# Kernel optimization log

Hardware: AMD Instinct MI355X
Metric: run time of the kernel (lower is better)

## Reference

```python
import jax, jax.numpy as jnp
import numpy as np

DQ_RATIO, DV_RATIO = 8, 2


def setup_inputs() -> dict:
    key = jax.random.key(0)
    k1, k2, k3, k4 = jax.random.split(key, 4)
    B, C, H, W = 16, 256, 64, 64
    dq, dv = C // DQ_RATIO, C // DV_RATIO
    imgs = jax.random.normal(k1, (B, C, H, W), dtype=jnp.float32)
    # small init keeps softmax logits in a sane range (like trained conv weights)
    w_qkv = jax.random.normal(k2, (2 * dq + dv, C), dtype=jnp.float32) * 0.02
    w_out = jax.random.normal(k3, (C, dv), dtype=jnp.float32) * 0.05
    scale = jax.random.normal(k4, (), dtype=jnp.float32)
    return {"imgs": imgs, "w_qkv": w_qkv, "w_out": w_out, "scale": scale}


def _maxpool2(x):
    # 2x2 max pool, stride 2; x: [b, c, h, w]
    b, c, h, w = x.shape
    return x.reshape(b, c, h // 2, 2, w // 2, 2).max(axis=(3, 5))


def reference(imgs, w_qkv, w_out, scale):
    b, c, h, w = imgs.shape
    dq, dv = c // DQ_RATIO, c // DV_RATIO
    # 1x1 conv == per-pixel channel matmul
    qkv = jnp.einsum('bchw,oc->bohw', imgs, w_qkv)
    q = qkv[:, :dq]                 # [b, dq, h, w]
    k = _maxpool2(qkv[:, dq:2 * dq])  # [b, dq, h/2, w/2]
    v = _maxpool2(qkv[:, 2 * dq:])    # [b, dv, h/2, w/2]
    q = q.reshape(b, dq, h * w)
    k = k.reshape(b, dq, (h * w) // 4)
    v = v.reshape(b, dv, (h * w) // 4)
    # attn[b, n, m] over downsampled kv positions m
    attn = jax.nn.softmax(jnp.einsum('bdn,bdm->bnm', q, k), axis=2)
    out = jnp.einsum('bdm,bnm->bdn', v, attn).reshape(b, dv, h, w)
    return imgs + jnp.einsum('bdhw,cd->bchw', out, w_out) * scale
```

## Files before the change

### kernel.cpp

```cpp
#include <hip/hip_runtime.h>

typedef __bf16 bf16;
typedef __bf16 bf16x2 __attribute__((ext_vector_type(2)));
typedef __bf16 bf16x4 __attribute__((ext_vector_type(4)));
typedef __bf16 bf16x8 __attribute__((ext_vector_type(8)));
typedef float f32x4 __attribute__((ext_vector_type(4)));

#define NB 16
#define NC 256
#define NHW 4096
#define NDQ 32
#define NDV 128
#define NM 1024

__global__ __launch_bounds__(256) void cvt_weights(const float* __restrict__ wq,
                                                   const float* __restrict__ wo,
                                                   bf16* __restrict__ wq16,
                                                   bf16* __restrict__ wo16) {
    int idx = blockIdx.x * 256 + threadIdx.x;
    const float* src;
    bf16* dst;
    int base;
    if (idx < 6144) { src = wq; dst = wq16; base = idx; }
    else            { src = wo; dst = wo16; base = idx - 6144; }
    float4 a = ((const float4*)src)[base * 2];
    float4 c = ((const float4*)src)[base * 2 + 1];
    bf16x8 v;
    v[0] = (bf16)a.x; v[1] = (bf16)a.y; v[2] = (bf16)a.z; v[3] = (bf16)a.w;
    v[4] = (bf16)c.x; v[5] = (bf16)c.y; v[6] = (bf16)c.z; v[7] = (bf16)c.w;
    *(bf16x8*)&dst[base * 8] = v;
}

__global__ __launch_bounds__(256) void qkv_mfma(const float* __restrict__ imgs,
                                                const bf16* __restrict__ wq16,
                                                bf16* __restrict__ qT,
                                                bf16* __restrict__ kT,
                                                bf16* __restrict__ vb) {
    __shared__ __align__(16) char lds[40960];
    bf16* XS = (bf16*)lds;
    bf16* WS = (bf16*)(lds + 16384);

    const int tid  = threadIdx.x;
    const int lane = tid & 63;
    const int w    = tid >> 6;
    const int lr   = lane & 15;
    const int lg   = lane >> 4;
    const int bx   = blockIdx.x;
    const int b    = blockIdx.y;
    const int n0   = bx * 128;

    f32x4 acc[3][8];
#pragma unroll
    for (int i = 0; i < 3; i++)
#pragma unroll
        for (int j = 0; j < 8; j++) acc[i][j] = (f32x4){0.f, 0.f, 0.f, 0.f};

    const int snl = tid & 63;
    const int scg = (tid >> 6) * 8;

    for (int kc = 0; kc < 4; kc++) {
        if (kc) __syncthreads();
#pragma unroll
        for (int j = 0; j < 4; j++) {
            int n  = snl + (j & 1) * 64;
            int c8 = scg + (j >> 1) * 32;
            const float* g = imgs + (size_t)(b * NC + kc * 64 + c8) * NHW + n0 + n;
            bf16x8 v;
#pragma unroll
            for (int i = 0; i < 8; i++) v[i] = (bf16)g[i * NHW];
            *(bf16x8*)(XS + n * 64 + ((((c8 >> 3) ^ (n & 7))) << 3)) = v;
        }
#pragma unroll
        for (int j = 0; j < 6; j++) {
            int idx = j * 256 + tid;
            int o = idx >> 3, s = idx & 7;
            bf16x8 v = *(const bf16x8*)(wq16 + (size_t)o * NC + kc * 64 + s * 8);
            *(bf16x8*)(WS + o * 64 + ((s ^ (o & 7)) << 3)) = v;
        }
        __syncthreads();
#pragma unroll
        for (int sub = 0; sub < 2; sub++) {
            bf16x8 af[3], bfr[8];
#pragma unroll
            for (int ot = 0; ot < 3; ot++) {
                int o = w * 48 + ot * 16 + lr;
                af[ot] = *(const bf16x8*)(WS + o * 64 + (((sub * 4 + lg) ^ (o & 7)) << 3));
            }
#pragma unroll
            for (int nt = 0; nt < 8; nt++) {
                int n = nt * 16 + lr;
                bfr[nt] = *(const bf16x8*)(XS + n * 64 + (((sub * 4 + lg) ^ (n & 7)) << 3));
            }
#pragma unroll
            for (int ot = 0; ot < 3; ot++)
#pragma unroll
                for (int nt = 0; nt < 8; nt++)
                    acc[ot][nt] = __builtin_amdgcn_mfma_f32_16x16x32_bf16(af[ot], bfr[nt], acc[ot][nt], 0, 0, 0);
        }
    }

#pragma unroll
    for (int ot = 0; ot < 3; ot++) {
        const int o_base = w * 48 + ot * 16;
        if (o_base < 32) {
            const int d0 = o_base + lg * 4;
#pragma unroll
            for (int nt = 0; nt < 8; nt++) {
                int n = n0 + nt * 16 + lr;
                bf16x4 v;
#pragma unroll
                for (int r = 0; r < 4; r++) v[r] = (bf16)acc[ot][nt][r];
                *(bf16x4*)&qT[((size_t)b * NHW + n) * NDQ + d0] = v;
            }
        } else {
            float pm[4][4];
#pragma unroll
            for (int ntg = 0; ntg < 4; ntg++)
#pragma unroll
                for (int r = 0; r < 4; r++) {
                    float v0 = fmaxf(acc[ot][ntg][r], acc[ot][ntg + 4][r]);
                    float v1 = __shfl_xor(v0, 1, 64);
                    pm[ntg][r] = fmaxf(v0, v1);
                }
            if (!(lr & 1)) {
                if (o_base < 64) {
                    const int d0 = o_base - 32 + lg * 4;
#pragma unroll
                    for (int ntg = 0; ntg < 4; ntg++) {
                        int m = bx * 32 + ((ntg * 16 + lr) >> 1);
                        bf16x4 v;
#pragma unroll
                        for (int r = 0; r < 4; r++) v[r] = (bf16)pm[ntg][r];
                        *(bf16x4*)&kT[((size_t)b * NM + m) * NDQ + d0] = v;
                    }
                } else {
                    const int dv0 = o_base - 64 + lg * 4;
#pragma unroll
                    for (int ntg = 0; ntg < 4; ntg++) {
                        int m = bx * 32 + ((ntg * 16 + lr) >> 1);
#pragma unroll
                        for (int r = 0; r < 4; r++)
                            vb[((size_t)b * NDV + dv0 + r) * NM + m] = (bf16)pm[ntg][r];
                    }
                }
            }
        }
    }
}

__global__ __launch_bounds__(256) void attn_mfma(const bf16* __restrict__ qT,
                                                 const bf16* __restrict__ kT,
                                                 const bf16* __restrict__ vb,
                                                 bf16* __restrict__ aT) {
    __shared__ __align__(16) char pool[37888];
    bf16* QT = (bf16*)pool;
    bf16* KT = (bf16*)(pool + 5120);
    bf16* VS = (bf16*)(pool + 10240);
    bf16* PS = (bf16*)(pool + 28672);
    float* DW = (float*)(pool + 28672);

    const int tid  = threadIdx.x;
    const int lane = tid & 63;
    const int w    = tid >> 6;
    const int lr   = lane & 15;
    const int lg   = lane >> 4;
    const int b    = blockIdx.y;
    const int n0   = blockIdx.x * 64;

    {
        const bf16* src = qT + (size_t)(b * NHW + n0 + (tid >> 2)) * NDQ + (tid & 3) * 8;
        *(bf16x8*)&QT[(tid >> 2) * 40 + (tid & 3) * 8] = *(const bf16x8*)src;
    }
    __syncthreads();

    bf16x8 QB[4];
#pragma unroll
    for (int nt = 0; nt < 4; nt++)
        QB[nt] = *(const bf16x8*)&QT[(nt * 16 + lr) * 40 + lg * 8];

    f32x4 zero = {0.f, 0.f, 0.f, 0.f};
    f32x4 acc[2][4];
#pragma unroll
    for (int dt = 0; dt < 2; dt++)
#pragma unroll
        for (int nt = 0; nt < 4; nt++) acc[dt][nt] = zero;
    float denp[4] = {0.f, 0.f, 0.f, 0.f};

    for (int t = 0; t < 16; t++) {
        const int m0 = t * 64;
        __syncthreads();
        {
            const bf16* src = kT + (size_t)(b * NM + m0 + (tid >> 2)) * NDQ + (tid & 3) * 8;
            *(bf16x8*)&KT[(tid >> 2) * 40 + (tid & 3) * 8] = *(const bf16x8*)src;
        }
        {
            const bf16* src = vb + (size_t)(b * NDV + (tid >> 1)) * NM + m0 + (tid & 1) * 32;
            bf16* dst = &VS[(tid >> 1) * 72 + (tid & 1) * 32];
#pragma unroll
            for (int u = 0; u < 4; u++)
                *(bf16x8*)(dst + u * 8) = *(const bf16x8*)(src + u * 8);
        }
        __syncthreads();

        bf16x8 ka = *(const bf16x8*)&KT[(w * 16 + lr) * 40 + lg * 8];
        f32x4 st[4];
#pragma unroll
        for (int nt = 0; nt < 4; nt++)
            st[nt] = __builtin_amdgcn_mfma_f32_16x16x32_bf16(ka, QB[nt], zero, 0, 0, 0);

#pragma unroll
        for (int nt = 0; nt < 4; nt++) {
            float e0 = __expf(st[nt][0]);
            float e1 = __expf(st[nt][1]);
            float e2 = __expf(st[nt][2]);
            float e3 = __expf(st[nt][3]);
            denp[nt] += (e0 + e1) + (e2 + e3);
            bf16x4 pv;
            pv[0] = (bf16)e0; pv[1] = (bf16)e1; pv[2] = (bf16)e2; pv[3] = (bf16)e3;
            *(bf16x4*)&PS[(nt * 16 + lr) * 72 + (w * 16 + lg * 4)] = pv;
        }
        __syncthreads();

#pragma unroll
        for (int mc = 0; mc < 2; mc++) {
            bf16x8 pb[4];
#pragma unroll
            for (int nt = 0; nt < 4; nt++)
                pb[nt] = *(const bf16x8*)&PS[(nt * 16 + lr) * 72 + mc * 32 + lg * 8];
#pragma unroll
            for (int dt = 0; dt < 2; dt++) {
                bf16x8 va = *(const bf16x8*)&VS[(w * 32 + dt * 16 + lr) * 72 + mc * 32 + lg * 8];
#pragma unroll
                for (int nt = 0; nt < 4; nt++)
                    acc[dt][nt] = __builtin_amdgcn_mfma_f32_16x16x32_bf16(va, pb[nt], acc[dt][nt], 0, 0, 0);
            }
        }
    }
    __syncthreads();

#pragma unroll
    for (int nt = 0; nt < 4; nt++) {
        denp[nt] += __shfl_xor(denp[nt], 16, 64);
        denp[nt] += __shfl_xor(denp[nt], 32, 64);
    }
    if (lane < 16) {
#pragma unroll
        for (int nt = 0; nt < 4; nt++) DW[(w * 4 + nt) * 16 + lane] = denp[nt];
    }
    __syncthreads();
    float rinv[4];
#pragma unroll
    for (int nt = 0; nt < 4; nt++) {
        float s = DW[(0 * 4 + nt) * 16 + lr] + DW[(1 * 4 + nt) * 16 + lr] +
                  DW[(2 * 4 + nt) * 16 + lr] + DW[(3 * 4 + nt) * 16 + lr];
        rinv[nt] = 1.0f / s;
    }

#pragma unroll
    for (int dt = 0; dt < 2; dt++)
#pragma unroll
        for (int nt = 0; nt < 4; nt++) {
            int d0 = w * 32 + dt * 16 + lg * 4;
            int n  = n0 + nt * 16 + lr;
            bf16x4 v;
#pragma unroll
            for (int r = 0; r < 4; r++) v[r] = (bf16)(acc[dt][nt][r] * rinv[nt]);
            *(bf16x4*)&aT[((size_t)b * NHW + n) * NDV + d0] = v;
        }
}

__global__ __launch_bounds__(256) void outproj_mfma(const bf16* __restrict__ aT,
                                                    const bf16* __restrict__ wo16,
                                                    const float* __restrict__ imgs,
                                                    const float* __restrict__ scale_p,
                                                    float* __restrict__ out) {
    __shared__ __align__(16) char lds[65536];
    bf16* XS = (bf16*)lds;
    bf16* WS = (bf16*)(lds + 32768);

    const int tid  = threadIdx.x;
    const int lane = tid & 63;
    const int w    = tid >> 6;
    const int lr   = lane & 15;
    const int lg   = lane >> 4;
    const int wr   = w >> 1, wc = w & 1;
    const int bx   = blockIdx.x;
    const int ch   = blockIdx.y;
    const int b    = blockIdx.z;
    const int n0   = bx * 128;

#pragma unroll
    for (int j = 0; j < 8; j++) {
        int idx = j * 256 + tid;
        int row = idx >> 4, s = idx & 15;
        int sw  = ((s ^ (row & 15)) << 3);
        *(bf16x8*)(XS + row * 128 + sw) =
            *(const bf16x8*)(aT + ((size_t)b * NHW + n0 + row) * NDV + s * 8);
        *(bf16x8*)(WS + row * 128 + sw) =
            *(const bf16x8*)(wo16 + (size_t)(ch * 128 + row) * NDV + s * 8);
    }
    __syncthreads();

    f32x4 acc[4][4];
#pragma unroll
    for (int i = 0; i < 4; i++)
#pragma unroll
        for (int j = 0; j < 4; j++) acc[i][j] = (f32x4){0.f, 0.f, 0.f, 0.f};

#pragma unroll
    for (int kk = 0; kk < 4; kk++) {
        bf16x8 af[4], bfr[4];
#pragma unroll
        for (int ot = 0; ot < 4; ot++) {
            int c = wr * 64 + ot * 16 + lr;
            af[ot] = *(const bf16x8*)(WS + c * 128 + (((kk * 4 + lg) ^ (c & 15)) << 3));
        }
#pragma unroll
        for (int nt = 0; nt < 4; nt++) {
            int n = wc * 64 + nt * 16 + lr;
            bfr[nt] = *(const bf16x8*)(XS + n * 128 + (((kk * 4 + lg) ^ (n & 15)) << 3));
        }
#pragma unroll
        for (int ot = 0; ot < 4; ot++)
#pragma unroll
            for (int nt = 0; nt < 4; nt++)
                acc[ot][nt] = __builtin_amdgcn_mfma_f32_16x16x32_bf16(af[ot], bfr[nt], acc[ot][nt], 0, 0, 0);
    }

    const float sc = *scale_p;
#pragma unroll
    for (int ot = 0; ot < 4; ot++)
#pragma unroll
        for (int nt = 0; nt < 4; nt++) {
            int n = n0 + wc * 64 + nt * 16 + lr;
#pragma unroll
            for (int r = 0; r < 4; r++) {
                int c = ch * 128 + wr * 64 + ot * 16 + lg * 4 + r;
                size_t off = ((size_t)b * NC + c) * NHW + n;
                out[off] = imgs[off] + sc * acc[ot][nt][r];
            }
        }
}

extern "C" void kernel_launch(void* const* d_in, const int* in_sizes, int n_in,
                              void* d_out, int out_size, void* d_ws, size_t ws_size,
                              hipStream_t stream) {
    const float* imgs  = (const float*)d_in[0];
    const float* w_qkv = (const float*)d_in[1];
    const float* w_out = (const float*)d_in[2];
    const float* scale = (const float*)d_in[3];
    float* out = (float*)d_out;

    char* wsb = (char*)d_ws;
    bf16* aTg  = (bf16*)(wsb);
    bf16* qTg  = (bf16*)(wsb + (16u << 20));
    bf16* kTg  = (bf16*)(wsb + (20u << 20));
    bf16* vbg  = (bf16*)(wsb + (21u << 20));
    bf16* wq16 = (bf16*)(wsb + (25u << 20));
    bf16* wo16 = (bf16*)(wsb + (25u << 20) + 98304);

    hipLaunchKernelGGL(cvt_weights, dim3(40), dim3(256), 0, stream,
                       w_qkv, w_out, wq16, wo16);
    hipLaunchKernelGGL(qkv_mfma, dim3(32, NB), dim3(256), 0, stream,
                       imgs, wq16, qTg, kTg, vbg);
    hipLaunchKernelGGL(attn_mfma, dim3(64, NB), dim3(256), 0, stream,
                       qTg, kTg, vbg, aTg);
    hipLaunchKernelGGL(outproj_mfma, dim3(32, 2, NB), dim3(256), 0, stream,
                       aTg, wo16, imgs, scale, out);
}
```

Before: 181.9 us.

## Retile qkv and attention kernels, prefetch K/V tiles into registers

The qkv projection kernel now covers 64 pixels per block (two half-row slices paired for the 2x2 pool), which doubles its grid for more parallelism and halves its accumulator registers. The attention kernel now handles 128 query pixels per block, so each K/V tile loaded is reused across twice as many queries. It also prefetches the next K/V tile into registers while the current one is computed, hiding global load latency. The costs are more LDS and registers in the attention kernel, which may lower occupancy, and fewer attention blocks.

```diff
diff --git a/kernel.cpp b/kernel.cpp
--- a/kernel.cpp
+++ b/kernel.cpp
@@ -36,9 +36,9 @@
                                                 bf16* __restrict__ qT,
                                                 bf16* __restrict__ kT,
                                                 bf16* __restrict__ vb) {
-    __shared__ __align__(16) char lds[40960];
+    __shared__ __align__(16) char lds[32768];
     bf16* XS = (bf16*)lds;
-    bf16* WS = (bf16*)(lds + 16384);
+    bf16* WS = (bf16*)(lds + 8192);
 
     const int tid  = threadIdx.x;
     const int lane = tid & 63;
@@ -46,29 +46,33 @@
     const int lr   = lane & 15;
     const int lg   = lane >> 4;
     const int bx   = blockIdx.x;
+    const int r    = bx >> 1;
+    const int half = bx & 1;
     const int b    = blockIdx.y;
-    const int n0   = bx * 128;
-
-    f32x4 acc[3][8];
+    const int nfb  = r * 128 + half * 32;
+
+    f32x4 acc[3][4];
 #pragma unroll
     for (int i = 0; i < 3; i++)
 #pragma unroll
-        for (int j = 0; j < 8; j++) acc[i][j] = (f32x4){0.f, 0.f, 0.f, 0.f};
+        for (int j = 0; j < 4; j++) acc[i][j] = (f32x4){0.f, 0.f, 0.f, 0.f};
 
     const int snl = tid & 63;
+    const int sg  = snl >> 5;
+    const int sc  = snl & 31;
     const int scg = (tid >> 6) * 8;
 
     for (int kc = 0; kc < 4; kc++) {
         if (kc) __syncthreads();
 #pragma unroll
-        for (int j = 0; j < 4; j++) {
-            int n  = snl + (j & 1) * 64;
-            int c8 = scg + (j >> 1) * 32;
-            const float* g = imgs + (size_t)(b * NC + kc * 64 + c8) * NHW + n0 + n;
+        for (int j = 0; j < 2; j++) {
+            int c8 = scg + j * 32;
+            const float* g = imgs + (size_t)(b * NC + kc * 64 + c8) * NHW
+                             + nfb + sg * 64 + sc;
             bf16x8 v;
 #pragma unroll
             for (int i = 0; i < 8; i++) v[i] = (bf16)g[i * NHW];
-            *(bf16x8*)(XS + n * 64 + ((((c8 >> 3) ^ (n & 7))) << 3)) = v;
+            *(bf16x8*)(XS + snl * 64 + ((((c8 >> 3) ^ (snl & 7))) << 3)) = v;
         }
 #pragma unroll
         for (int j = 0; j < 6; j++) {
@@ -80,21 +84,21 @@
         __syncthreads();
 #pragma unroll
         for (int sub = 0; sub < 2; sub++) {
-            bf16x8 af[3], bfr[8];
+            bf16x8 af[3], bfr[4];
 #pragma unroll
             for (int ot = 0; ot < 3; ot++) {
                 int o = w * 48 + ot * 16 + lr;
                 af[ot] = *(const bf16x8*)(WS + o * 64 + (((sub * 4 + lg) ^ (o & 7)) << 3));
             }
 #pragma unroll
-            for (int nt = 0; nt < 8; nt++) {
+            for (int nt = 0; nt < 4; nt++) {
                 int n = nt * 16 + lr;
                 bfr[nt] = *(const bf16x8*)(XS + n * 64 + (((sub * 4 + lg) ^ (n & 7)) << 3));
             }
 #pragma unroll
             for (int ot = 0; ot < 3; ot++)
 #pragma unroll
-                for (int nt = 0; nt < 8; nt++)
+                for (int nt = 0; nt < 4; nt++)
                     acc[ot][nt] = __builtin_amdgcn_mfma_f32_16x16x32_bf16(af[ot], bfr[nt], acc[ot][nt], 0, 0, 0);
         }
     }
@@ -105,42 +109,42 @@
         if (o_base < 32) {
             const int d0 = o_base + lg * 4;
 #pragma unroll
-            for (int nt = 0; nt < 8; nt++) {
-                int n = n0 + nt * 16 + lr;
+            for (int nt = 0; nt < 4; nt++) {
+                int n = nfb + (nt >> 1) * 64 + (nt & 1) * 16 + lr;
                 bf16x4 v;
 #pragma unroll
-                for (int r = 0; r < 4; r++) v[r] = (bf16)acc[ot][nt][r];
+                for (int rr = 0; rr < 4; rr++) v[rr] = (bf16)acc[ot][nt][rr];
                 *(bf16x4*)&qT[((size_t)b * NHW + n) * NDQ + d0] = v;
             }
         } else {
-            float pm[4][4];
-#pragma unroll
-            for (int ntg = 0; ntg < 4; ntg++)
-#pragma unroll
-                for (int r = 0; r < 4; r++) {
-                    float v0 = fmaxf(acc[ot][ntg][r], acc[ot][ntg + 4][r]);
+            float pm[2][4];
+#pragma unroll
+            for (int nt = 0; nt < 2; nt++)
+#pragma unroll
+                for (int rr = 0; rr < 4; rr++) {
+                    float v0 = fmaxf(acc[ot][nt][rr], acc[ot][nt + 2][rr]);
                     float v1 = __shfl_xor(v0, 1, 64);
-                    pm[ntg][r] = fmaxf(v0, v1);
+                    pm[nt][rr] = fmaxf(v0, v1);
                 }
             if (!(lr & 1)) {
                 if (o_base < 64) {
                     const int d0 = o_base - 32 + lg * 4;
 #pragma unroll
-                    for (int ntg = 0; ntg < 4; ntg++) {
-                        int m = bx * 32 + ((ntg * 16 + lr) >> 1);
+                    for (int nt = 0; nt < 2; nt++) {
+                        int m = r * 32 + half * 16 + nt * 8 + (lr >> 1);
                         bf16x4 v;
 #pragma unroll
-                        for (int r = 0; r < 4; r++) v[r] = (bf16)pm[ntg][r];
+                        for (int rr = 0; rr < 4; rr++) v[rr] = (bf16)pm[nt][rr];
                         *(bf16x4*)&kT[((size_t)b * NM + m) * NDQ + d0] = v;
                     }
                 } else {
                     const int dv0 = o_base - 64 + lg * 4;
 #pragma unroll
-                    for (int ntg = 0; ntg < 4; ntg++) {
-                        int m = bx * 32 + ((ntg * 16 + lr) >> 1);
-#pragma unroll
-                        for (int r = 0; r < 4; r++)
-                            vb[((size_t)b * NDV + dv0 + r) * NM + m] = (bf16)pm[ntg][r];
+                    for (int nt = 0; nt < 2; nt++) {
+                        int m = r * 32 + half * 16 + nt * 8 + (lr >> 1);
+#pragma unroll
+                        for (int rr = 0; rr < 4; rr++)
+                            vb[((size_t)b * NDV + dv0 + rr) * NM + m] = (bf16)pm[nt][rr];
                     }
                 }
             }
@@ -152,12 +156,12 @@
                                                  const bf16* __restrict__ kT,
                                                  const bf16* __restrict__ vb,
                                                  bf16* __restrict__ aT) {
-    __shared__ __align__(16) char pool[37888];
+    __shared__ __align__(16) char pool[52224];
     bf16* QT = (bf16*)pool;
-    bf16* KT = (bf16*)(pool + 5120);
-    bf16* VS = (bf16*)(pool + 10240);
-    bf16* PS = (bf16*)(pool + 28672);
-    float* DW = (float*)(pool + 28672);
+    bf16* KT = (bf16*)(pool + 10240);
+    bf16* VS = (bf16*)(pool + 15360);
+    bf16* PS = (bf16*)(pool + 33792);
+    float* DW = (float*)(pool + 33792);
 
     const int tid  = threadIdx.x;
     const int lane = tid & 63;
@@ -165,51 +169,61 @@
     const int lr   = lane & 15;
     const int lg   = lane >> 4;
     const int b    = blockIdx.y;
-    const int n0   = blockIdx.x * 64;
+    const int n0   = blockIdx.x * 128;
 
     {
-        const bf16* src = qT + (size_t)(b * NHW + n0 + (tid >> 2)) * NDQ + (tid & 3) * 8;
-        *(bf16x8*)&QT[(tid >> 2) * 40 + (tid & 3) * 8] = *(const bf16x8*)src;
-    }
+        const int row = tid >> 1, off = (tid & 1) * 16;
+        const bf16* src = qT + (size_t)(b * NHW + n0 + row) * NDQ + off;
+        *(bf16x8*)&QT[row * 40 + off]     = *(const bf16x8*)src;
+        *(bf16x8*)&QT[row * 40 + off + 8] = *(const bf16x8*)(src + 8);
+    }
+
+    const int krow = tid >> 2, koff = (tid & 3) * 8;
+    const int vrow = tid >> 1, vmb  = (tid & 1) * 32;
+    bf16x8 krg, vrg[4];
+    krg = *(const bf16x8*)(kT + (size_t)(b * NM + krow) * NDQ + koff);
+#pragma unroll
+    for (int u = 0; u < 4; u++)
+        vrg[u] = *(const bf16x8*)(vb + (size_t)(b * NDV + vrow) * NM + vmb + u * 8);
+
     __syncthreads();
 
-    bf16x8 QB[4];
-#pragma unroll
-    for (int nt = 0; nt < 4; nt++)
+    bf16x8 QB[8];
+#pragma unroll
+    for (int nt = 0; nt < 8; nt++)
         QB[nt] = *(const bf16x8*)&QT[(nt * 16 + lr) * 40 + lg * 8];
 
     f32x4 zero = {0.f, 0.f, 0.f, 0.f};
-    f32x4 acc[2][4];
+    f32x4 acc[2][8];
 #pragma unroll
     for (int dt = 0; dt < 2; dt++)
 #pragma unroll
-        for (int nt = 0; nt < 4; nt++) acc[dt][nt] = zero;
-    float denp[4] = {0.f, 0.f, 0.f, 0.f};
+        for (int nt = 0; nt < 8; nt++) acc[dt][nt] = zero;
+    float denp[8] = {0.f, 0.f, 0.f, 0.f, 0.f, 0.f, 0.f, 0.f};
 
     for (int t = 0; t < 16; t++) {
-        const int m0 = t * 64;
+        if (t) __syncthreads();
+        *(bf16x8*)&KT[krow * 40 + koff] = krg;
+#pragma unroll
+        for (int u = 0; u < 4; u++)
+            *(bf16x8*)&VS[vrow * 72 + vmb + u * 8] = vrg[u];
+        if (t < 15) {
+            const int m1 = (t + 1) * 64;
+            krg = *(const bf16x8*)(kT + (size_t)(b * NM + m1 + krow) * NDQ + koff);
+#pragma unroll
+            for (int u = 0; u < 4; u++)
+                vrg[u] = *(const bf16x8*)(vb + (size_t)(b * NDV + vrow) * NM + m1 + vmb + u * 8);
+        }
         __syncthreads();
-        {
-            const bf16* src = kT + (size_t)(b * NM + m0 + (tid >> 2)) * NDQ + (tid & 3) * 8;
-            *(bf16x8*)&KT[(tid >> 2) * 40 + (tid & 3) * 8] = *(const bf16x8*)src;
-        }
-        {
-            const bf16* src = vb + (size_t)(b * NDV + (tid >> 1)) * NM + m0 + (tid & 1) * 32;
-            bf16* dst = &VS[(tid >> 1) * 72 + (tid & 1) * 32];
-#pragma unroll
-            for (int u = 0; u < 4; u++)
-                *(bf16x8*)(dst + u * 8) = *(const bf16x8*)(src + u * 8);
-        }
-        __syncthreads();
 
         bf16x8 ka = *(const bf16x8*)&KT[(w * 16 + lr) * 40 + lg * 8];
-        f32x4 st[4];
-#pragma unroll
-        for (int nt = 0; nt < 4; nt++)
+        f32x4 st[8];
+#pragma unroll
+        for (int nt = 0; nt < 8; nt++)
             st[nt] = __builtin_amdgcn_mfma_f32_16x16x32_bf16(ka, QB[nt], zero, 0, 0, 0);
 
 #pragma unroll
-        for (int nt = 0; nt < 4; nt++) {
+        for (int nt = 0; nt < 8; nt++) {
             float e0 = __expf(st[nt][0]);
             float e1 = __expf(st[nt][1]);
             float e2 = __expf(st[nt][2]);
@@ -223,15 +237,15 @@
 
 #pragma unroll
         for (int mc = 0; mc < 2; mc++) {
-            bf16x8 pb[4];
-#pragma unroll
-            for (int nt = 0; nt < 4; nt++)
+            bf16x8 pb[8];
+#pragma unroll
+            for (int nt = 0; nt < 8; nt++)
                 pb[nt] = *(const bf16x8*)&PS[(nt * 16 + lr) * 72 + mc * 32 + lg * 8];
 #pragma unroll
             for (int dt = 0; dt < 2; dt++) {
                 bf16x8 va = *(const bf16x8*)&VS[(w * 32 + dt * 16 + lr) * 72 + mc * 32 + lg * 8];
 #pragma unroll
-                for (int nt = 0; nt < 4; nt++)
+                for (int nt = 0; nt < 8; nt++)
                     acc[dt][nt] = __builtin_amdgcn_mfma_f32_16x16x32_bf16(va, pb[nt], acc[dt][nt], 0, 0, 0);
             }
         }
@@ -239,32 +253,32 @@
     __syncthreads();
 
 #pragma unroll
-    for (int nt = 0; nt < 4; nt++) {
+    for (int nt = 0; nt < 8; nt++) {
         denp[nt] += __shfl_xor(denp[nt], 16, 64);
         denp[nt] += __shfl_xor(denp[nt], 32, 64);
     }
     if (lane < 16) {
 #pragma unroll
-        for (int nt = 0; nt < 4; nt++) DW[(w * 4 + nt) * 16 + lane] = denp[nt];
+        for (int nt = 0; nt < 8; nt++) DW[(w * 8 + nt) * 16 + lane] = denp[nt];
     }
     __syncthreads();
-    float rinv[4];
-#pragma unroll
-    for (int nt = 0; nt < 4; nt++) {
-        float s = DW[(0 * 4 + nt) * 16 + lr] + DW[(1 * 4 + nt) * 16 + lr] +
-                  DW[(2 * 4 + nt) * 16 + lr] + DW[(3 * 4 + nt) * 16 + lr];
+    float rinv[8];
+#pragma unroll
+    for (int nt = 0; nt < 8; nt++) {
+        float s = DW[(0 * 8 + nt) * 16 + lr] + DW[(1 * 8 + nt) * 16 + lr] +
+                  DW[(2 * 8 + nt) * 16 + lr] + DW[(3 * 8 + nt) * 16 + lr];
         rinv[nt] = 1.0f / s;
     }
 
 #pragma unroll
     for (int dt = 0; dt < 2; dt++)
 #pragma unroll
-        for (int nt = 0; nt < 4; nt++) {
+        for (int nt = 0; nt < 8; nt++) {
             int d0 = w * 32 + dt * 16 + lg * 4;
             int n  = n0 + nt * 16 + lr;
             bf16x4 v;
 #pragma unroll
-            for (int r = 0; r < 4; r++) v[r] = (bf16)(acc[dt][nt][r] * rinv[nt]);
+            for (int rr = 0; rr < 4; rr++) v[rr] = (bf16)(acc[dt][nt][rr] * rinv[nt]);
             *(bf16x4*)&aT[((size_t)b * NHW + n) * NDV + d0] = v;
         }
 }
@@ -334,10 +348,10 @@
         for (int nt = 0; nt < 4; nt++) {
             int n = n0 + wc * 64 + nt * 16 + lr;
 #pragma unroll
-            for (int r = 0; r < 4; r++) {
-                int c = ch * 128 + wr * 64 + ot * 16 + lg * 4 + r;
+            for (int rr = 0; rr < 4; rr++) {
+                int c = ch * 128 + wr * 64 + ot * 16 + lg * 4 + rr;
                 size_t off = ((size_t)b * NC + c) * NHW + n;
-                out[off] = imgs[off] + sc * acc[ot][nt][r];
+                out[off] = imgs[off] + sc * acc[ot][nt][rr];
             }
         }
 }
@@ -361,9 +375,9 @@
 
     hipLaunchKernelGGL(cvt_weights, dim3(40), dim3(256), 0, stream,
                        w_qkv, w_out, wq16, wo16);
-    hipLaunchKernelGGL(qkv_mfma, dim3(32, NB), dim3(256), 0, stream,
+    hipLaunchKernelGGL(qkv_mfma, dim3(64, NB), dim3(256), 0, stream,
                        imgs, wq16, qTg, kTg, vbg);
-    hipLaunchKernelGGL(attn_mfma, dim3(64, NB), dim3(256), 0, stream,
+    hipLaunchKernelGGL(attn_mfma, dim3(32, NB), dim3(256), 0, stream,
                        qTg, kTg, vbg, aTg);
     hipLaunchKernelGGL(outproj_mfma, dim3(32, 2, NB), dim3(256), 0, stream,
                        aTg, wo16, imgs, scale, out);
```

After: 191.0 us. +5.0%, slower.
